# Kernel tuning notes

Measured on AMD Instinct MI355X. Metric: run time of the kernel, lower is better.

## Reference

```python
import jax, jax.numpy as jnp
import numpy as np
from jax import lax

GAP_PENALTY = 0.0
TEMPERATURE = 1.0
B, A, L, D, K = 64, 26, 384, 512, 18


def setup_inputs() -> dict:
    key = jax.random.key(0)
    k1, k2, k3, k4 = jax.random.split(key, 4)
    matrices = jax.random.normal(k1, (B, A, L), dtype=jnp.float32)
    # ragged lengths: (len_i, len_0) per pair, in [L//2, L]
    shapes = jax.random.randint(k2, (B, 2), L // 2, L + 1, dtype=jnp.int32)
    s = 1.0 / np.sqrt(A * K)  # torch Conv1d default init scale
    conv_w = jax.random.uniform(k3, (D, A, K), minval=-s, maxval=s, dtype=jnp.float32)
    conv_b = jax.random.uniform(k4, (D,), minval=-s, maxval=s, dtype=jnp.float32)
    return {"matrices": matrices, "shapes": shapes, "conv_w": conv_w, "conv_b": conv_b}


def _smoothmax3(a, b, c, t):
    # t * log(exp(a/t) + exp(b/t) + exp(c/t)), numerically stable
    m = jnp.maximum(jnp.maximum(a, b), c)
    return m + t * jnp.log(jnp.exp((a - m) / t) + jnp.exp((b - m) / t) + jnp.exp((c - m) / t))


def _nw_matrix(sim, t, g):
    # sim: (L, L). Returns smoothed NW value matrix V: (L+1, L+1).
    # V[i,j] = sim[i-1,j-1] + smoothmax(V[i-1,j-1], V[i-1,j]-g, V[i,j-1]-g)
    n = sim.shape[0]
    row0 = -g * jnp.arange(n + 1, dtype=sim.dtype)  # free/affine leading gaps on top row

    def row_step(prev_row, inp):
        s_row, i = inp  # s_row: (L,)
        v_left0 = -g * i  # V[i, 0]

        def col_step(left, xs):
            s, diag, up = xs
            v = s + _smoothmax3(diag, up - g, left - g, t)
            return v, v

        _, rest = lax.scan(col_step, v_left0, (s_row, prev_row[:-1], prev_row[1:]))
        new_row = jnp.concatenate([v_left0[None], rest])
        return new_row, new_row

    _, rows = lax.scan(row_step, row0, (sim, jnp.arange(1, n + 1, dtype=sim.dtype)))
    return jnp.concatenate([row0[None], rows], axis=0)


def needleman_wunsch(sim, shapes, gap_penalty, temperature):
    # sim: (B, L, L) similarity vs sequence 0; shapes: (B, 2) int lengths.
    # Soft alignment posterior = grad of smoothed terminal score wrt similarity.
    li = jnp.clip(shapes[:, 0], 0, sim.shape[1])
    lj = jnp.clip(shapes[:, 1], 0, sim.shape[2])

    def total_score(s):
        V = jax.vmap(lambda m: _nw_matrix(m, temperature, gap_penalty))(s)  # (B, L+1, L+1)
        b = jnp.arange(s.shape[0])
        return jnp.sum(V[b, li, lj])

    return jax.grad(total_score)(sim)  # (B, L, L), expected match matrix


def reference(matrices, shapes, conv_w, conv_b):
    # Conv1d padding='same' with even kernel: torch pads (k-1)//2 left, k//2 right
    k = conv_w.shape[-1]
    pad = ((k - 1) // 2, k // 2)
    emb = lax.conv_general_dilated(
        matrices, conv_w, window_strides=(1,), padding=[pad],
        dimension_numbers=("NCH", "OIH", "NCH"),
    ) + conv_b[None, :, None]  # (B, D, L)
    e = jnp.transpose(emb, (0, 2, 1))  # (B, L, D)
    sim = jnp.einsum("bld,md->blm", e, e[0])  # (B, L_i, L_0): similarity vs sequence 0
    align = needleman_wunsch(sim, shapes, GAP_PENALTY, TEMPERATURE)  # (B, L, L)
    m = jnp.transpose(matrices, (0, 2, 1))  # (B, L, A)
    # consensus in sequence-0 coordinates, then project back to each sequence
    consensus = jnp.mean(jnp.einsum("nia,nij->nja", m, align), axis=0)  # (L, A)
    return jnp.einsum("ja,nij->nia", consensus, align)  # (B, L, A)
```

## Files before the change

kernel.cpp:

```cpp
#include <hip/hip_runtime.h>
#include <hip/hip_bf16.h>
#include <math.h>

#define B_  64
#define A_  26
#define L_  384
#define D_  512
#define K_  18
#define SZD 245760

typedef __attribute__((ext_vector_type(8))) short bf16x8;
typedef __attribute__((ext_vector_type(4))) float f32x4;
typedef unsigned short ushort_t;
typedef unsigned int uint_t;

__device__ __forceinline__ void stD(float* sp, int z, int c, float v) {
    int dl = z / 6, dr = z - dl * 6;
    sp[(size_t)(dl + (c >> 2)) * 1536 + dr * 256 + dl * 4 + (c & 3)] = v;
}

__device__ __forceinline__ ushort_t f2bf(float v) {
    uint_t u = __float_as_uint(v);
    uint_t r = (u + 0x7FFFu + ((u >> 16) & 1u)) >> 16;
    return (ushort_t)r;
}

__global__ void transpose_w_kernel(const float* __restrict__ w, float* __restrict__ wt) {
    int o = blockIdx.x * blockDim.x + threadIdx.x;
    int total = A_ * K_ * D_;
    if (o >= total) return;
    int d = o % D_;
    int r = o / D_;
    wt[o] = w[(size_t)d * (A_ * K_) + r];
}

__global__ __launch_bounds__(512) void conv_kernel(const float* __restrict__ x,
                                                   const float* __restrict__ wt,
                                                   const float* __restrict__ bias,
                                                   ushort_t* __restrict__ ehi,
                                                   ushort_t* __restrict__ elo) {
    const int TL = 32;
    const int XW = TL + K_ - 1;
    int l0 = blockIdx.x * TL;
    int b  = blockIdx.y;
    int d  = threadIdx.x;
    __shared__ float xs[A_][XW];
    for (int idx = threadIdx.x; idx < A_ * XW; idx += 512) {
        int a = idx / XW, p = idx % XW;
        int g = l0 - (K_ - 1) / 2 + p;
        xs[a][p] = (g >= 0 && g < L_) ? x[((size_t)b * A_ + a) * L_ + g] : 0.0f;
    }
    __syncthreads();
    float acc[TL];
#pragma unroll
    for (int l = 0; l < TL; ++l) acc[l] = 0.0f;
#pragma unroll 1
    for (int a = 0; a < A_; ++a) {
        float xr[XW];
#pragma unroll
        for (int p = 0; p < XW; ++p) xr[p] = xs[a][p];
        const float* wrow = wt + (size_t)(a * K_) * D_ + d;
#pragma unroll
        for (int k = 0; k < K_; ++k) {
            float w = wrow[(size_t)k * D_];
#pragma unroll
            for (int l = 0; l < TL; ++l)
                acc[l] = fmaf(xr[k + l], w, acc[l]);
        }
    }
    float bv = bias[d];
#pragma unroll
    for (int l = 0; l < TL; ++l) {
        float v = acc[l] + bv;
        ushort_t h = f2bf(v);
        float hf = __uint_as_float(((uint_t)h) << 16);
        ushort_t lo = f2bf(v - hf);
        size_t idx = ((size_t)b * L_ + (l0 + l)) * D_ + d;
        ehi[idx] = h;
        elo[idx] = lo;
    }
}

__global__ __launch_bounds__(256) void sim_kernel(const ushort_t* __restrict__ ehi,
                                                  const ushort_t* __restrict__ elo,
                                                  float* __restrict__ simD) {
    int b = blockIdx.z;
    int w = threadIdx.x >> 6;
    int lane = threadIdx.x & 63;
    int l0 = blockIdx.y * 64 + 32 * (w >> 1);
    int m0 = blockIdx.x * 64 + 32 * (w & 1);
    int r = lane & 15, g = lane >> 4;
    size_t rowA = ((size_t)b * L_ + l0 + r) * D_ + g * 8;
    size_t rowB = ((size_t)m0 + r) * D_ + g * 8;
    const ushort_t* pah = ehi + rowA;
    const ushort_t* pal = elo + rowA;
    const ushort_t* pbh = ehi + rowB;
    const ushort_t* pbl = elo + rowB;
    f32x4 acc00 = {0.f, 0.f, 0.f, 0.f}, acc01 = acc00, acc10 = acc00, acc11 = acc00;
#pragma unroll 2
    for (int ks = 0; ks < 16; ++ks) {
        int off = ks * 32;
        bf16x8 Ah0 = *(const bf16x8*)(pah + off);
        bf16x8 Ah1 = *(const bf16x8*)(pah + 16 * D_ + off);
        bf16x8 Al0 = *(const bf16x8*)(pal + off);
        bf16x8 Al1 = *(const bf16x8*)(pal + 16 * D_ + off);
        bf16x8 Bh0 = *(const bf16x8*)(pbh + off);
        bf16x8 Bh1 = *(const bf16x8*)(pbh + 16 * D_ + off);
        bf16x8 Bl0 = *(const bf16x8*)(pbl + off);
        bf16x8 Bl1 = *(const bf16x8*)(pbl + 16 * D_ + off);
        acc00 = __builtin_amdgcn_mfma_f32_16x16x32_bf16(Ah0, Bh0, acc00, 0, 0, 0);
        acc00 = __builtin_amdgcn_mfma_f32_16x16x32_bf16(Ah0, Bl0, acc00, 0, 0, 0);
        acc00 = __builtin_amdgcn_mfma_f32_16x16x32_bf16(Al0, Bh0, acc00, 0, 0, 0);
        acc01 = __builtin_amdgcn_mfma_f32_16x16x32_bf16(Ah0, Bh1, acc01, 0, 0, 0);
        acc01 = __builtin_amdgcn_mfma_f32_16x16x32_bf16(Ah0, Bl1, acc01, 0, 0, 0);
        acc01 = __builtin_amdgcn_mfma_f32_16x16x32_bf16(Al0, Bh1, acc01, 0, 0, 0);
        acc10 = __builtin_amdgcn_mfma_f32_16x16x32_bf16(Ah1, Bh0, acc10, 0, 0, 0);
        acc10 = __builtin_amdgcn_mfma_f32_16x16x32_bf16(Ah1, Bl0, acc10, 0, 0, 0);
        acc10 = __builtin_amdgcn_mfma_f32_16x16x32_bf16(Al1, Bh0, acc10, 0, 0, 0);
        acc11 = __builtin_amdgcn_mfma_f32_16x16x32_bf16(Ah1, Bh1, acc11, 0, 0, 0);
        acc11 = __builtin_amdgcn_mfma_f32_16x16x32_bf16(Ah1, Bl1, acc11, 0, 0, 0);
        acc11 = __builtin_amdgcn_mfma_f32_16x16x32_bf16(Al1, Bh1, acc11, 0, 0, 0);
    }
    float* sp = simD + (size_t)b * SZD;
#pragma unroll
    for (int v = 0; v < 4; ++v) {
        int ar0 = l0 + g * 4 + v, ar1 = ar0 + 16;
        int ac0 = m0 + r,         ac1 = ac0 + 16;
        stD(sp, ar0, ac0, acc00[v]);
        stD(sp, ar0, ac1, acc01[v]);
        stD(sp, ar1, ac0, acc10[v]);
        stD(sp, ar1, ac1, acc11[v]);
    }
}

__global__ __launch_bounds__(256, 1) void nw_fwd_kernel(const float* __restrict__ simD, float* __restrict__ VD) {
    int b = blockIdx.x;
    int tid = threadIdx.x;
    int w = tid >> 6, l = tid & 63;
    __shared__ float4 MA[4][64], MB4[4][64], MC[4][64];
    __shared__ int FL[4];
    const float4 Z4 = {0.f, 0.f, 0.f, 0.f};
    for (int k = tid; k < 256; k += 256) {
        int s = k >> 6, ll = k & 63;
        MA[s][ll] = Z4; MB4[s][ll] = Z4; MC[s][ll] = Z4;
    }
    if (tid < 4) FL[tid] = (tid == 3) ? -1 : -1000000;
    __syncthreads();
    volatile int* flg = FL;
    const float* pS = simD + (size_t)b * SZD + l * 4;
    float*       pV = VD   + (size_t)b * SZD + l * 4;
    float4 buf[6];
#pragma unroll
    for (int r = 0; r < 6; ++r) buf[r] = *(const float4*)(pS + w * 1536 + r * 256);
    int lm = (l == 0) ? 0 : (l - 1);
#pragma unroll 1
    for (int T = w; T < 159; T += 4) {
        int sp = (T - 1) & 3;
        while (flg[sp] != T - 1) {}
        asm volatile("" ::: "memory");
        float4 Ar = MA[sp][l];
        float4 Bs = MB4[sp][l];
        float4 Cs = MC[sp][l];
        float4 Bn = MB4[sp][lm];
        float4 Cn = MC[sp][lm];
        if (l == 0) { Bn = Z4; Cn = Z4; }
        float vleft[6] = {Ar.x, Ar.y, Ar.z, Ar.w, Bs.x, Bs.y};
        float d0 = Bn.z;
        float uin[4] = {Cn.x, Cn.y, Cn.z, Cn.w};
        float sc[6][4];
#pragma unroll
        for (int r = 0; r < 6; ++r) {
            sc[r][0] = buf[r].x; sc[r][1] = buf[r].y; sc[r][2] = buf[r].z; sc[r][3] = buf[r].w;
        }
        int dP = min(T + 4, 158);
#pragma unroll
        for (int r = 0; r < 6; ++r) buf[r] = *(const float4*)(pS + dP * 1536 + r * 256);
        int ct = T - l;
        float nbc[4] = {0.f, 0.f, 0.f, 0.f}, nbp = 0.f;
        if (ct >= 0 && ct <= 95) {
            float vout[6][4];
#pragma unroll
            for (int q = 0; q < 4; ++q) {
                float dg = (q == 0) ? d0 : uin[q - 1];
                float up = uin[q];
#pragma unroll
                for (int r = 0; r < 6; ++r) {
                    float lf = vleft[r];
                    float mx = fmaxf(dg, fmaxf(up, lf));
                    float v = sc[r][q] + mx + __logf(__expf(dg - mx) + __expf(up - mx) + __expf(lf - mx));
                    dg = lf; up = v;
                    vleft[r] = v;
                    vout[r][q] = v;
                }
            }
            nbp = Cs.w;
#pragma unroll
            for (int q = 0; q < 4; ++q) nbc[q] = vout[5][q];
            float* pVd = pV + (size_t)T * 1536;
#pragma unroll
            for (int r = 0; r < 6; ++r) {
                float4 t;
                t.x = vout[r][0]; t.y = vout[r][1]; t.z = vout[r][2]; t.w = vout[r][3];
                *(float4*)(pVd + r * 256) = t;
            }
        }
        float4 pa; pa.x = vleft[0]; pa.y = vleft[1]; pa.z = vleft[2]; pa.w = vleft[3];
        float4 pb; pb.x = vleft[4]; pb.y = vleft[5]; pb.z = nbp; pb.w = 0.f;
        float4 pc; pc.x = nbc[0]; pc.y = nbc[1]; pc.z = nbc[2]; pc.w = nbc[3];
        MA[w][l] = pa; MB4[w][l] = pb; MC[w][l] = pc;
        asm volatile("s_waitcnt lgkmcnt(0)" ::: "memory");
        if (l == 0) flg[w] = T;
    }
}

__global__ __launch_bounds__(256, 1) void nw_bwd_kernel(const float* __restrict__ simD,
                                                        const float* __restrict__ VD,
                                                        const int* __restrict__ shapes,
                                                        float* __restrict__ ED) {
    int b = blockIdx.x;
    int tid = threadIdx.x;
    int w = tid >> 6, l = tid & 63;
    __shared__ float4 MA[4][64], MB4[4][64], MC[4][64], MD[4][64], MEx[4][64], MF[4][64];
    __shared__ int FL[4];
    const float4 Z4 = {0.f, 0.f, 0.f, 0.f};
    for (int k = tid; k < 256; k += 256) {
        int s = k >> 6, ll = k & 63;
        MA[s][ll] = Z4; MB4[s][ll] = Z4; MC[s][ll] = Z4;
        MD[s][ll] = Z4; MEx[s][ll] = Z4; MF[s][ll] = Z4;
    }
    if (tid < 4) FL[tid] = (tid == 3) ? -1 : -1000000;
    __syncthreads();
    volatile int* flg = FL;
    const float* pS = simD + (size_t)b * SZD + l * 4;
    const float* pV = VD   + (size_t)b * SZD + l * 4;
    float*       pE = ED   + (size_t)b * SZD + l * 4;
    int li = min(max(shapes[2 * b + 0], 0), L_);
    int lj = min(max(shapes[2 * b + 1], 0), L_);
    float4 bufV[6], bufS[6];
#pragma unroll
    for (int r = 0; r < 6; ++r) {
        bufV[r] = *(const float4*)(pV + (158 - w) * 1536 + r * 256);
        bufS[r] = *(const float4*)(pS + (158 - w) * 1536 + r * 256);
    }
    int lp = (l == 63) ? 63 : (l + 1);
#pragma unroll 1
    for (int T = w; T < 159; T += 4) {
        int sp = (T - 1) & 3;
        while (flg[sp] != T - 1) {}
        asm volatile("" ::: "memory");
        float4 Ar = MA[sp][l];
        float4 Br = MB4[sp][l];
        float4 Cr = MC[sp][l];
        float4 Dn = MD[sp][lp];
        float4 En = MEx[sp][lp];
        float4 Fn = MF[sp][lp];
        if (l == 63) { Dn = Z4; En = Z4; Fn = Z4; }
        float e[6] = {Ar.x, Ar.y, Ar.z, Ar.w, Br.x, Br.y};
        float u[6] = {Br.z, Br.w, Cr.x, Cr.y, Cr.z, Cr.w};
        float enb_c[4] = {Dn.x, Dn.y, Dn.z, Dn.w};
        float unb_c[4] = {En.x, En.y, En.z, En.w};
        float enbtd_s = Fn.x, unbtd_s = Fn.y;
        float e0r = e[0], u0r = u[0];
        float Vq[6][4], Sq[6][4];
#pragma unroll
        for (int r = 0; r < 6; ++r) {
            Vq[r][0] = bufV[r].x; Vq[r][1] = bufV[r].y; Vq[r][2] = bufV[r].z; Vq[r][3] = bufV[r].w;
            Sq[r][0] = bufS[r].x; Sq[r][1] = bufS[r].y; Sq[r][2] = bufS[r].z; Sq[r][3] = bufS[r].w;
        }
        int dP = max(158 - (T + 4), 0);
#pragma unroll
        for (int r = 0; r < 6; ++r) {
            bufV[r] = *(const float4*)(pV + dP * 1536 + r * 256);
            bufS[r] = *(const float4*)(pS + dP * 1536 + r * 256);
        }
        int ct = 158 - T - l;
        float necar[4] = {0.f, 0.f, 0.f, 0.f}, nucar[4] = {0.f, 0.f, 0.f, 0.f};
        if (ct >= 0 && ct <= 95) {
            float Eo[6][4];
#pragma unroll
            for (int qq = 0; qq < 4; ++qq) {
                const int q = 3 - qq;
                int j = 4 * ct + q + 1;
                bool jlt = (j < L_);
                float eo[6], uo[6];
#pragma unroll
                for (int r = 0; r < 6; ++r) { eo[r] = e[r]; uo[r] = u[r]; }
#pragma unroll
                for (int rr = 0; rr < 6; ++rr) {
                    const int r = 5 - rr;
                    int i = 6 * l + r + 1;
                    bool ilt = (i < L_);
                    float Vv = Vq[r][q];
                    float u_new = Vv - Sq[r][q];
                    float eb_old, ub_old, eb_new, ub_new;
                    if (r == 5) {
                        eb_old = (q == 3) ? enbtd_s : enb_c[q + 1];
                        ub_old = (q == 3) ? unbtd_s : unb_c[q + 1];
                        eb_new = enb_c[q];
                        ub_new = unb_c[q];
                    } else {
                        eb_old = eo[r + 1]; ub_old = uo[r + 1];
                        eb_new = e[r + 1];  ub_new = u[r + 1];
                    }
                    float wtd = (ilt && jlt) ? __expf(Vv - ub_old) : 0.f;
                    float wtu = ilt ? __expf(Vv - ub_new) : 0.f;
                    float wtl = jlt ? __expf(Vv - uo[r]) : 0.f;
                    float en = (i == li && j == lj) ? 1.f : 0.f;
                    en += wtd * eb_old + wtu * eb_new + wtl * eo[r];
                    e[r] = en; u[r] = u_new;
                    Eo[r][q] = en;
                }
            }
#pragma unroll
            for (int q = 0; q < 4; ++q) {
                necar[q] = Eo[0][q];
                nucar[q] = Vq[0][q] - Sq[0][q];
            }
            float* pEd = pE + (size_t)(158 - T) * 1536;
#pragma unroll
            for (int r = 0; r < 6; ++r) {
                float4 t;
                t.x = Eo[r][0]; t.y = Eo[r][1]; t.z = Eo[r][2]; t.w = Eo[r][3];
                *(float4*)(pEd + r * 256) = t;
            }
        }
        float4 pa; pa.x = e[0]; pa.y = e[1]; pa.z = e[2]; pa.w = e[3];
        float4 pb; pb.x = e[4]; pb.y = e[5]; pb.z = u[0]; pb.w = u[1];
        float4 pc; pc.x = u[2]; pc.y = u[3]; pc.z = u[4]; pc.w = u[5];
        float4 pd; pd.x = necar[0]; pd.y = necar[1]; pd.z = necar[2]; pd.w = necar[3];
        float4 pe; pe.x = nucar[0]; pe.y = nucar[1]; pe.z = nucar[2]; pe.w = nucar[3];
        float4 pf; pf.x = e0r; pf.y = u0r; pf.z = 0.f; pf.w = 0.f;
        MA[w][l] = pa; MB4[w][l] = pb; MC[w][l] = pc;
        MD[w][l] = pd; MEx[w][l] = pe; MF[w][l] = pf;
        asm volatile("s_waitcnt lgkmcnt(0)" ::: "memory");
        if (l == 0) flg[w] = T;
    }
}

__global__ __launch_bounds__(256) void consensus_kernel(const float* __restrict__ x,
                                                        const float* __restrict__ ED,
                                                        float* __restrict__ cons) {
    int n  = blockIdx.y;
    int j0 = blockIdx.x * 64;
    __shared__ float ms[A_][L_];
    for (int idx = threadIdx.x; idx < A_ * L_; idx += 256)
        ((float*)ms)[idx] = x[(size_t)n * A_ * L_ + idx];
    __syncthreads();
    int jl = threadIdx.x & 63;
    int g  = threadIdx.x >> 6;
    int a0 = g * 7;
    int na = (a0 + 7 <= A_) ? 7 : (A_ - a0);
    int j  = j0 + jl;
    float acc[7] = {0.f, 0.f, 0.f, 0.f, 0.f, 0.f, 0.f};
    const float* aB = ED + (size_t)n * SZD + (j >> 2) * 1536 + (j & 3);
#pragma unroll 1
    for (int dl = 0; dl < 64; ++dl) {
        const float* ap = aB + dl * 1540;
#pragma unroll
        for (int dr = 0; dr < 6; ++dr) {
            float al = ap[dr * 256];
            int i = dl * 6 + dr;
#pragma unroll
            for (int t = 0; t < 7; ++t)
                if (t < na) acc[t] = fmaf(al, ms[a0 + t][i], acc[t]);
        }
    }
    for (int t = 0; t < na; ++t)
        atomicAdd(&cons[(size_t)j * A_ + a0 + t], acc[t] * (1.0f / B_));
}

__global__ __launch_bounds__(256) void out_kernel(const float* __restrict__ ED,
                                                  const float* __restrict__ cons,
                                                  float* __restrict__ out) {
    int n  = blockIdx.y;
    int i0 = blockIdx.x * 32;
    __shared__ float cs[L_][A_];
    __shared__ float as_[32][L_ + 1];
    for (int idx = threadIdx.x; idx < L_ * A_; idx += 256)
        ((float*)cs)[idx] = cons[idx];
    const float* aB = ED + (size_t)n * SZD;
    for (int idx = threadIdx.x; idx < 32 * L_; idx += 256) {
        int r = idx / L_, c = idx - r * L_;
        int z = i0 + r;
        int dl = z / 6, dr = z - dl * 6;
        as_[r][c] = aB[(size_t)(dl + (c >> 2)) * 1536 + dr * 256 + dl * 4 + (c & 3)];
    }
    __syncthreads();
    for (int o = threadIdx.x; o < 32 * A_; o += 256) {
        int il = o / A_, a = o % A_;
        float s = 0.f;
        for (int jj = 0; jj < L_; ++jj)
            s = fmaf(as_[il][jj], cs[jj][a], s);
        out[((size_t)n * L_ + i0 + il) * A_ + a] = s;
    }
}

extern "C" void kernel_launch(void* const* d_in, const int* in_sizes, int n_in,
                              void* d_out, int out_size, void* d_ws, size_t ws_size,
                              hipStream_t stream) {
    const float* matrices = (const float*)d_in[0];
    const int*   shapes   = (const int*)d_in[1];
    const float* conv_w   = (const float*)d_in[2];
    const float* conv_b   = (const float*)d_in[3];
    float* out = (float*)d_out;

    char* p = (char*)d_ws;
    float*    ED  = (float*)p;
    ushort_t* ehi = (ushort_t*)p;
    ushort_t* elo = ehi + (size_t)B_ * L_ * D_;
    float* simD = (float*)(p + (size_t)B_ * SZD * 4);
    float* VD   = simD + (size_t)B_ * SZD;
    float* wt   = VD + (size_t)B_ * SZD;
    float* cons = wt + (size_t)A_ * K_ * D_;

    transpose_w_kernel<<<(A_ * K_ * D_ + 255) / 256, 256, 0, stream>>>(conv_w, wt);
    conv_kernel<<<dim3(L_ / 32, B_), 512, 0, stream>>>(matrices, wt, conv_b, ehi, elo);
    sim_kernel<<<dim3(L_ / 64, L_ / 64, B_), 256, 0, stream>>>(ehi, elo, simD);
    nw_fwd_kernel<<<B_, 256, 0, stream>>>(simD, VD);
    nw_bwd_kernel<<<B_, 256, 0, stream>>>(simD, VD, shapes, ED);
    hipMemsetAsync(cons, 0, (size_t)L_ * A_ * sizeof(float), stream);
    consensus_kernel<<<dim3(L_ / 64, B_), 256, 0, stream>>>(matrices, ED, cons);
    out_kernel<<<dim3(L_ / 32, B_), 256, 0, stream>>>(ED, cons, out);
}
```

Measured before the change: 988.6 us.

## Recast conv as im2col split-bf16 MFMA GEMM and repack alignment to row-major

Replaces the scalar FP32 direct convolution with an im2col pass and a split-bf16 (hi/lo, three products) MFMA matrix multiply whose K dimension is padded to 480. The weights are split into bf16 hi/lo once per call. A repack kernel is also added that converts the diagonal-layout alignment matrix into natural row-major layout, so the consensus and output kernels read it contiguously. The trade-offs are extra workspace traffic for the im2col buffers and the repack, plus a small loss of precision from the bf16x3 emulation of FP32.

```diff
diff --git a/kernel.cpp b/kernel.cpp
--- a/kernel.cpp
+++ b/kernel.cpp
@@ -7,6 +7,8 @@
 #define L_  384
 #define D_  512
 #define K_  18
+#define KC  480
+#define LL  147456
 #define SZD 245760
 
 typedef __attribute__((ext_vector_type(8))) short bf16x8;
@@ -25,59 +27,99 @@
     return (ushort_t)r;
 }
 
-__global__ void transpose_w_kernel(const float* __restrict__ w, float* __restrict__ wt) {
+__global__ void wsplit_kernel(const float* __restrict__ w, ushort_t* __restrict__ wh,
+                              ushort_t* __restrict__ wl) {
     int o = blockIdx.x * blockDim.x + threadIdx.x;
-    int total = A_ * K_ * D_;
-    if (o >= total) return;
-    int d = o % D_;
-    int r = o / D_;
-    wt[o] = w[(size_t)d * (A_ * K_) + r];
-}
-
-__global__ __launch_bounds__(512) void conv_kernel(const float* __restrict__ x,
-                                                   const float* __restrict__ wt,
-                                                   const float* __restrict__ bias,
-                                                   ushort_t* __restrict__ ehi,
-                                                   ushort_t* __restrict__ elo) {
-    const int TL = 32;
-    const int XW = TL + K_ - 1;
-    int l0 = blockIdx.x * TL;
+    if (o >= D_ * KC) return;
+    int d = o / KC, r = o - d * KC;
+    float v = (r < A_ * K_) ? w[(size_t)d * (A_ * K_) + r] : 0.0f;
+    ushort_t h = f2bf(v);
+    float hf = __uint_as_float(((uint_t)h) << 16);
+    wh[o] = h;
+    wl[o] = f2bf(v - hf);
+}
+
+__global__ __launch_bounds__(256) void im2col_kernel(const float* __restrict__ x,
+                                                     ushort_t* __restrict__ xh,
+                                                     ushort_t* __restrict__ xl) {
     int b  = blockIdx.y;
-    int d  = threadIdx.x;
-    __shared__ float xs[A_][XW];
-    for (int idx = threadIdx.x; idx < A_ * XW; idx += 512) {
-        int a = idx / XW, p = idx % XW;
-        int g = l0 - (K_ - 1) / 2 + p;
-        xs[a][p] = (g >= 0 && g < L_) ? x[((size_t)b * A_ + a) * L_ + g] : 0.0f;
-    }
-    __syncthreads();
-    float acc[TL];
-#pragma unroll
-    for (int l = 0; l < TL; ++l) acc[l] = 0.0f;
-#pragma unroll 1
-    for (int a = 0; a < A_; ++a) {
-        float xr[XW];
-#pragma unroll
-        for (int p = 0; p < XW; ++p) xr[p] = xs[a][p];
-        const float* wrow = wt + (size_t)(a * K_) * D_ + d;
-#pragma unroll
-        for (int k = 0; k < K_; ++k) {
-            float w = wrow[(size_t)k * D_];
-#pragma unroll
-            for (int l = 0; l < TL; ++l)
-                acc[l] = fmaf(xr[k + l], w, acc[l]);
-        }
-    }
-    float bv = bias[d];
-#pragma unroll
-    for (int l = 0; l < TL; ++l) {
-        float v = acc[l] + bv;
+    int lt = blockIdx.x;
+    const float* xb = x + (size_t)b * A_ * L_;
+    for (int idx = threadIdx.x; idx < 64 * KC; idx += 256) {
+        int l = lt * 64 + idx / KC;
+        int r = idx % KC;
+        float v = 0.0f;
+        if (r < A_ * K_) {
+            int a = r / K_, kk = r - a * K_;
+            int g = l + kk - 8;
+            if (g >= 0 && g < L_) v = xb[(size_t)a * L_ + g];
+        }
         ushort_t h = f2bf(v);
         float hf = __uint_as_float(((uint_t)h) << 16);
-        ushort_t lo = f2bf(v - hf);
-        size_t idx = ((size_t)b * L_ + (l0 + l)) * D_ + d;
-        ehi[idx] = h;
-        elo[idx] = lo;
+        size_t o = ((size_t)b * L_ + l) * KC + r;
+        xh[o] = h;
+        xl[o] = f2bf(v - hf);
+    }
+}
+
+__global__ __launch_bounds__(256) void convmm_kernel(const ushort_t* __restrict__ xh,
+                                                     const ushort_t* __restrict__ xl,
+                                                     const ushort_t* __restrict__ wh,
+                                                     const ushort_t* __restrict__ wl,
+                                                     const float* __restrict__ bias,
+                                                     ushort_t* __restrict__ ehi,
+                                                     ushort_t* __restrict__ elo) {
+    int b = blockIdx.z;
+    int w = threadIdx.x >> 6;
+    int lane = threadIdx.x & 63;
+    int l0 = blockIdx.y * 64 + 32 * (w >> 1);
+    int d0 = blockIdx.x * 64 + 32 * (w & 1);
+    int r = lane & 15, g = lane >> 4;
+    const ushort_t* pah = xh + ((size_t)b * L_ + l0 + r) * KC + g * 8;
+    const ushort_t* pal = xl + ((size_t)b * L_ + l0 + r) * KC + g * 8;
+    const ushort_t* pbh = wh + (size_t)(d0 + r) * KC + g * 8;
+    const ushort_t* pbl = wl + (size_t)(d0 + r) * KC + g * 8;
+    f32x4 acc00 = {0.f, 0.f, 0.f, 0.f}, acc01 = acc00, acc10 = acc00, acc11 = acc00;
+#pragma unroll 3
+    for (int ks = 0; ks < 15; ++ks) {
+        int off = ks * 32;
+        bf16x8 Ah0 = *(const bf16x8*)(pah + off);
+        bf16x8 Ah1 = *(const bf16x8*)(pah + 16 * KC + off);
+        bf16x8 Al0 = *(const bf16x8*)(pal + off);
+        bf16x8 Al1 = *(const bf16x8*)(pal + 16 * KC + off);
+        bf16x8 Bh0 = *(const bf16x8*)(pbh + off);
+        bf16x8 Bh1 = *(const bf16x8*)(pbh + 16 * KC + off);
+        bf16x8 Bl0 = *(const bf16x8*)(pbl + off);
+        bf16x8 Bl1 = *(const bf16x8*)(pbl + 16 * KC + off);
+        acc00 = __builtin_amdgcn_mfma_f32_16x16x32_bf16(Ah0, Bh0, acc00, 0, 0, 0);
+        acc00 = __builtin_amdgcn_mfma_f32_16x16x32_bf16(Ah0, Bl0, acc00, 0, 0, 0);
+        acc00 = __builtin_amdgcn_mfma_f32_16x16x32_bf16(Al0, Bh0, acc00, 0, 0, 0);
+        acc01 = __builtin_amdgcn_mfma_f32_16x16x32_bf16(Ah0, Bh1, acc01, 0, 0, 0);
+        acc01 = __builtin_amdgcn_mfma_f32_16x16x32_bf16(Ah0, Bl1, acc01, 0, 0, 0);
+        acc01 = __builtin_amdgcn_mfma_f32_16x16x32_bf16(Al0, Bh1, acc01, 0, 0, 0);
+        acc10 = __builtin_amdgcn_mfma_f32_16x16x32_bf16(Ah1, Bh0, acc10, 0, 0, 0);
+        acc10 = __builtin_amdgcn_mfma_f32_16x16x32_bf16(Ah1, Bl0, acc10, 0, 0, 0);
+        acc10 = __builtin_amdgcn_mfma_f32_16x16x32_bf16(Al1, Bh0, acc10, 0, 0, 0);
+        acc11 = __builtin_amdgcn_mfma_f32_16x16x32_bf16(Ah1, Bh1, acc11, 0, 0, 0);
+        acc11 = __builtin_amdgcn_mfma_f32_16x16x32_bf16(Ah1, Bl1, acc11, 0, 0, 0);
+        acc11 = __builtin_amdgcn_mfma_f32_16x16x32_bf16(Al1, Bh1, acc11, 0, 0, 0);
+    }
+#pragma unroll
+    for (int v = 0; v < 4; ++v) {
+        int lr0 = l0 + g * 4 + v, lr1 = lr0 + 16;
+        int dc0 = d0 + r,         dc1 = dc0 + 16;
+        float vals[4] = {acc00[v] + bias[dc0], acc01[v] + bias[dc1],
+                         acc10[v] + bias[dc0], acc11[v] + bias[dc1]};
+        int lrs[4] = {lr0, lr0, lr1, lr1};
+        int dcs[4] = {dc0, dc1, dc0, dc1};
+#pragma unroll
+        for (int t = 0; t < 4; ++t) {
+            ushort_t h = f2bf(vals[t]);
+            float hf = __uint_as_float(((uint_t)h) << 16);
+            size_t o = ((size_t)b * L_ + lrs[t]) * D_ + dcs[t];
+            ehi[o] = h;
+            elo[o] = f2bf(vals[t] - hf);
+        }
     }
 }
 
@@ -337,8 +379,25 @@
     }
 }
 
+__global__ __launch_bounds__(256) void repack_kernel(const float* __restrict__ ED,
+                                                     float* __restrict__ Enat) {
+    int n  = blockIdx.y;
+    int jt = blockIdx.x;
+    int jl = threadIdx.x & 63;
+    int gp = threadIdx.x >> 6;
+    int j  = jt * 64 + jl;
+    const float* eb = ED + (size_t)n * SZD + (j >> 2) * 1536 + (j & 3);
+    float* ob = Enat + (size_t)n * LL + j;
+#pragma unroll 4
+    for (int i = gp * 96; i < gp * 96 + 96; ++i) {
+        int dl = i / 6, dr = i - dl * 6;
+        float v = eb[(size_t)dl * 1540 + dr * 256];
+        ob[(size_t)i * L_] = v;
+    }
+}
+
 __global__ __launch_bounds__(256) void consensus_kernel(const float* __restrict__ x,
-                                                        const float* __restrict__ ED,
+                                                        const float* __restrict__ Enat,
                                                         float* __restrict__ cons) {
     int n  = blockIdx.y;
     int j0 = blockIdx.x * 64;
@@ -352,24 +411,18 @@
     int na = (a0 + 7 <= A_) ? 7 : (A_ - a0);
     int j  = j0 + jl;
     float acc[7] = {0.f, 0.f, 0.f, 0.f, 0.f, 0.f, 0.f};
-    const float* aB = ED + (size_t)n * SZD + (j >> 2) * 1536 + (j & 3);
-#pragma unroll 1
-    for (int dl = 0; dl < 64; ++dl) {
-        const float* ap = aB + dl * 1540;
-#pragma unroll
-        for (int dr = 0; dr < 6; ++dr) {
-            float al = ap[dr * 256];
-            int i = dl * 6 + dr;
-#pragma unroll
-            for (int t = 0; t < 7; ++t)
-                if (t < na) acc[t] = fmaf(al, ms[a0 + t][i], acc[t]);
-        }
+    const float* aE = Enat + (size_t)n * LL + j;
+    for (int i = 0; i < L_; ++i) {
+        float al = aE[(size_t)i * L_];
+#pragma unroll
+        for (int t = 0; t < 7; ++t)
+            if (t < na) acc[t] = fmaf(al, ms[a0 + t][i], acc[t]);
     }
     for (int t = 0; t < na; ++t)
         atomicAdd(&cons[(size_t)j * A_ + a0 + t], acc[t] * (1.0f / B_));
 }
 
-__global__ __launch_bounds__(256) void out_kernel(const float* __restrict__ ED,
+__global__ __launch_bounds__(256) void out_kernel(const float* __restrict__ Enat,
                                                   const float* __restrict__ cons,
                                                   float* __restrict__ out) {
     int n  = blockIdx.y;
@@ -378,12 +431,10 @@
     __shared__ float as_[32][L_ + 1];
     for (int idx = threadIdx.x; idx < L_ * A_; idx += 256)
         ((float*)cs)[idx] = cons[idx];
-    const float* aB = ED + (size_t)n * SZD;
+    const float* aE = Enat + (size_t)n * LL;
     for (int idx = threadIdx.x; idx < 32 * L_; idx += 256) {
         int r = idx / L_, c = idx - r * L_;
-        int z = i0 + r;
-        int dl = z / 6, dr = z - dl * 6;
-        as_[r][c] = aB[(size_t)(dl + (c >> 2)) * 1536 + dr * 256 + dl * 4 + (c & 3)];
+        as_[r][c] = aE[(size_t)(i0 + r) * L_ + c];
     }
     __syncthreads();
     for (int o = threadIdx.x; o < 32 * A_; o += 256) {
@@ -405,20 +456,31 @@
     float* out = (float*)d_out;
 
     char* p = (char*)d_ws;
-    float*    ED  = (float*)p;
+    float*    EDiag = (float*)p;
+    ushort_t* xh = (ushort_t*)p;
+    ushort_t* xl = xh + (size_t)B_ * L_ * KC;
+    p += (size_t)B_ * SZD * 4;
     ushort_t* ehi = (ushort_t*)p;
     ushort_t* elo = ehi + (size_t)B_ * L_ * D_;
-    float* simD = (float*)(p + (size_t)B_ * SZD * 4);
-    float* VD   = simD + (size_t)B_ * SZD;
-    float* wt   = VD + (size_t)B_ * SZD;
-    float* cons = wt + (size_t)A_ * K_ * D_;
-
-    transpose_w_kernel<<<(A_ * K_ * D_ + 255) / 256, 256, 0, stream>>>(conv_w, wt);
-    conv_kernel<<<dim3(L_ / 32, B_), 512, 0, stream>>>(matrices, wt, conv_b, ehi, elo);
+    p += (size_t)B_ * L_ * D_ * 4;
+    float* simD = (float*)p;
+    float* Enat = simD;
+    p += (size_t)B_ * SZD * 4;
+    float* VD = (float*)p;
+    p += (size_t)B_ * SZD * 4;
+    ushort_t* wh = (ushort_t*)p;
+    ushort_t* wl = wh + (size_t)D_ * KC;
+    p += (size_t)D_ * KC * 4;
+    float* cons = (float*)p;
+
+    wsplit_kernel<<<(D_ * KC + 255) / 256, 256, 0, stream>>>(conv_w, wh, wl);
+    im2col_kernel<<<dim3(L_ / 64, B_), 256, 0, stream>>>(matrices, xh, xl);
+    convmm_kernel<<<dim3(D_ / 64, L_ / 64, B_), 256, 0, stream>>>(xh, xl, wh, wl, conv_b, ehi, elo);
     sim_kernel<<<dim3(L_ / 64, L_ / 64, B_), 256, 0, stream>>>(ehi, elo, simD);
     nw_fwd_kernel<<<B_, 256, 0, stream>>>(simD, VD);
-    nw_bwd_kernel<<<B_, 256, 0, stream>>>(simD, VD, shapes, ED);
+    nw_bwd_kernel<<<B_, 256, 0, stream>>>(simD, VD, shapes, EDiag);
+    repack_kernel<<<dim3(L_ / 64, B_), 256, 0, stream>>>(EDiag, Enat);
     hipMemsetAsync(cons, 0, (size_t)L_ * A_ * sizeof(float), stream);
-    consensus_kernel<<<dim3(L_ / 64, B_), 256, 0, stream>>>(matrices, ED, cons);
-    out_kernel<<<dim3(L_ / 32, B_), 256, 0, stream>>>(ED, cons, out);
-}
+    consensus_kernel<<<dim3(L_ / 64, B_), 256, 0, stream>>>(matrices, Enat, cons);
+    out_kernel<<<dim3(L_ / 32, B_), 256, 0, stream>>>(Enat, cons, out);
+}
```

Result: slower. 1.017 ms (+2.9%).
